# Performance work log

Measured on AMD Instinct MI355X. Metric: run time of the kernel, lower is better.

Reference implementation:

```python
import jax, jax.numpy as jnp
import numpy as np

GRID_H, GRID_W = 32, 32
THRESHOLD = 1.0
SMOOTH = 0.5


def setup_inputs() -> dict:
    key = jax.random.key(0)
    x = jax.random.normal(key, (64, GRID_H * GRID_W, 768), dtype=jnp.float32)
    return {"x": x}


def reference(x) -> jnp.ndarray:
    B, N, D = x.shape
    H, W = GRID_H, GRID_W
    xr = x.reshape(B, H, W, D)

    # L2 norm of neighbor differences (same as torch.norm(diff, dim=-1))
    diff_h = xr[:, :, 1:, :] - xr[:, :, :-1, :]            # [B, H, W-1, D]
    diff_v = xr[:, 1:, :, :] - xr[:, :-1, :, :]            # [B, H-1, W, D]
    anomaly_h = jnp.sqrt(jnp.sum(diff_h * diff_h, axis=-1))  # [B, H, W-1]
    anomaly_v = jnp.sqrt(jnp.sum(diff_v * diff_v, axis=-1))  # [B, H-1, W]

    # Torch code uses .any() over the batch dim: a patch is anomalous for ALL
    # batch elements if ANY batch element exceeds the threshold.
    exceed_h = jnp.any(anomaly_h > THRESHOLD, axis=0)      # [H, W-1]
    exceed_v = jnp.any(anomaly_v > THRESHOLD, axis=0)      # [H-1, W]

    # Interior patches: i in [1, H-2], j in [1, W-2].
    # Conditions checked per (i, j): ah[i, j-1], ah[i, j], av[i-1, j], av[i, j]
    mask = (exceed_h[1:H - 1, 0:W - 2]
            | exceed_h[1:H - 1, 1:W - 1]
            | exceed_v[0:H - 2, 1:W - 1]
            | exceed_v[1:H - 1, 1:W - 1])                  # [H-2, W-2]

    # 4-neighbor average (all reads from the ORIGINAL xr, as in the torch code)
    avg = (xr[:, 0:H - 2, 1:W - 1, :] + xr[:, 2:H, 1:W - 1, :]
           + xr[:, 1:H - 1, 0:W - 2, :] + xr[:, 1:H - 1, 2:W, :]) * 0.25

    center = xr[:, 1:H - 1, 1:W - 1, :]
    blended = (1.0 - SMOOTH) * center + SMOOTH * avg
    interior = jnp.where(mask[None, :, :, None], blended, center)

    out = xr.at[:, 1:H - 1, 1:W - 1, :].set(interior)
    return out.reshape(B, N, D)
```

## Files before the change

### kernel.cpp

```cpp
#include <hip/hip_runtime.h>

#define THRESH 1.0f

typedef float nfloat4 __attribute__((ext_vector_type(4)));

__device__ __forceinline__ float sqdiff4(float4 a, float4 b) {
  float dx = a.x - b.x, dy = a.y - b.y, dz = a.z - b.z, dw = a.w - b.w;
  return dx * dx + dy * dy + dz * dz + dw * dw;
}

__global__ __launch_bounds__(192) void mask_kernel(
    const float* __restrict__ x, int* __restrict__ mask) {
  const int n = blockIdx.x;
  const int i = n >> 5, j = n & 31;
  const int t = threadIdx.x;
  if (i < 1 || i > 30 || j < 1 || j > 30) {
    if (t == 0) mask[n] = 0;
    return;
  }
  __shared__ float red[3][4];
  __shared__ int sdone;
  if (t == 0) sdone = 0;
  __syncthreads();
  const int lane = t & 63;
  const int wid = t >> 6;
  const float4* xv = (const float4*)x;

  for (int b = 0; b < 64; ++b) {
    const size_t base = ((size_t)b * 1024 + n) * 192 + t;
    float4 c = xv[base];
    float4 l = xv[base - 192];
    float4 r = xv[base + 192];
    float4 u = xv[base - 32 * 192];
    float4 d = xv[base + 32 * 192];
    float sl = sqdiff4(c, l);
    float sr = sqdiff4(r, c);
    float su = sqdiff4(c, u);
    float sd = sqdiff4(d, c);
#pragma unroll
    for (int off = 32; off > 0; off >>= 1) {
      sl += __shfl_down(sl, off, 64);
      sr += __shfl_down(sr, off, 64);
      su += __shfl_down(su, off, 64);
      sd += __shfl_down(sd, off, 64);
    }
    if (lane == 0) {
      red[wid][0] = sl; red[wid][1] = sr;
      red[wid][2] = su; red[wid][3] = sd;
    }
    __syncthreads();
    if (t == 0) {
      float L = red[0][0] + red[1][0] + red[2][0];
      float R = red[0][1] + red[1][1] + red[2][1];
      float U = red[0][2] + red[1][2] + red[2][2];
      float D = red[0][3] + red[1][3] + red[2][3];
      if (L > THRESH || R > THRESH || U > THRESH || D > THRESH) sdone = 1;
    }
    __syncthreads();
    if (sdone) break;
  }
  if (t == 0) mask[n] = sdone;
}

__global__ __launch_bounds__(192) void apply_kernel(
    const float* __restrict__ x, const int* __restrict__ mask,
    float* __restrict__ out) {
  const int orig = blockIdx.x;
  const int bn = (orig & 7) * 8192 + (orig >> 3);
  const int n = bn & 1023;
  const int t = threadIdx.x;
  const size_t base = (size_t)bn * 192 + t;
  const float4* xv = (const float4*)x;
  nfloat4* ov = (nfloat4*)out;

  float4 c = xv[base];
  float4 res = c;
  if (mask[n]) {
    float4 l = xv[base - 192];
    float4 r = xv[base + 192];
    float4 u = xv[base - 32 * 192];
    float4 d = xv[base + 32 * 192];
    res.x = 0.5f * c.x + 0.125f * ((l.x + r.x) + (u.x + d.x));
    res.y = 0.5f * c.y + 0.125f * ((l.y + r.y) + (u.y + d.y));
    res.z = 0.5f * c.z + 0.125f * ((l.z + r.z) + (u.z + d.z));
    res.w = 0.5f * c.w + 0.125f * ((l.w + r.w) + (u.w + d.w));
  }
  nfloat4 nres = {res.x, res.y, res.z, res.w};
  __builtin_nontemporal_store(nres, ov + base);
}

extern "C" void kernel_launch(void* const* d_in, const int* in_sizes, int n_in,
                              void* d_out, int out_size, void* d_ws,
                              size_t ws_size, hipStream_t stream) {
  const float* x = (const float*)d_in[0];
  float* out = (float*)d_out;
  int* mask = (int*)d_ws;

  mask_kernel<<<1024, 192, 0, stream>>>(x, mask);
  apply_kernel<<<64 * 1024, 192, 0, stream>>>(x, mask, out);
}
```

Measured before the change: 348.2 us.

## Stream apply kernel down rows with register and shared-memory neighbor reuse

```diff
diff --git a/kernel.cpp b/kernel.cpp
--- a/kernel.cpp
+++ b/kernel.cpp
@@ -7,6 +7,11 @@
 __device__ __forceinline__ float sqdiff4(float4 a, float4 b) {
   float dx = a.x - b.x, dy = a.y - b.y, dz = a.z - b.z, dw = a.w - b.w;
   return dx * dx + dy * dy + dz * dz + dw * dw;
+}
+
+__device__ __forceinline__ nfloat4 to_n(float4 v) {
+  nfloat4 r = {v.x, v.y, v.z, v.w};
+  return r;
 }
 
 __global__ __launch_bounds__(192) void mask_kernel(
@@ -62,31 +67,104 @@
   if (t == 0) mask[n] = sdone;
 }
 
-__global__ __launch_bounds__(192) void apply_kernel(
+__global__ __launch_bounds__(512) void apply_kernel(
     const float* __restrict__ x, const int* __restrict__ mask,
     float* __restrict__ out) {
   const int orig = blockIdx.x;
-  const int bn = (orig & 7) * 8192 + (orig >> 3);
-  const int n = bn & 1023;
-  const int t = threadIdx.x;
-  const size_t base = (size_t)bn * 192 + t;
+  const int bn = (orig & 7) * 32 + (orig >> 3);
+  const int b  = bn >> 2;
+  const int jg = bn & 3;
+  const int t  = threadIdx.x;
+  const int cl = t >> 6;
+  const int k  = t & 63;
+  const int jglob = jg * 8 + cl;
+
+  __shared__ float4 row[10 * 192];
+
   const float4* xv = (const float4*)x;
   nfloat4* ov = (nfloat4*)out;
 
-  float4 c = xv[base];
-  float4 res = c;
-  if (mask[n]) {
-    float4 l = xv[base - 192];
-    float4 r = xv[base + 192];
-    float4 u = xv[base - 32 * 192];
-    float4 d = xv[base + 32 * 192];
-    res.x = 0.5f * c.x + 0.125f * ((l.x + r.x) + (u.x + d.x));
-    res.y = 0.5f * c.y + 0.125f * ((l.y + r.y) + (u.y + d.y));
-    res.z = 0.5f * c.z + 0.125f * ((l.z + r.z) + (u.z + d.z));
-    res.w = 0.5f * c.w + 0.125f * ((l.w + r.w) + (u.w + d.w));
+  const size_t batch_base = (size_t)b * 1024 * 192;
+  const int jL = (jg == 0) ? 0 : jg * 8 - 1;
+  const int jR = (jg == 3) ? 31 : jg * 8 + 8;
+  const bool haloT = (t < 384);
+  const int hj   = (t < 192) ? jL : jR;
+  const int hoff = (t < 192) ? t : (t - 192);
+  const int hslot = (t < 192) ? hoff : (9 * 192 + hoff);
+
+  float4 rU0, rU1, rU2, rC0, rC1, rC2, rD0, rD1, rD2, rN0, rN1, rN2;
+  float4 hC = {0, 0, 0, 0}, hN = {0, 0, 0, 0};
+
+  auto rowbase = [&](int i) -> size_t {
+    return batch_base + (size_t)(i * 32 + jglob) * 192 + k;
+  };
+  auto halobase = [&](int i) -> size_t {
+    return batch_base + (size_t)(i * 32 + hj) * 192 + hoff;
+  };
+
+  {
+    const size_t b0 = rowbase(0), b1 = rowbase(1), b2 = rowbase(2);
+    rU0 = xv[b0]; rU1 = xv[b0 + 64]; rU2 = xv[b0 + 128];
+    rC0 = xv[b1]; rC1 = xv[b1 + 64]; rC2 = xv[b1 + 128];
+    rD0 = xv[b2]; rD1 = xv[b2 + 64]; rD2 = xv[b2 + 128];
+    if (haloT) hC = xv[halobase(1)];
+    __builtin_nontemporal_store(to_n(rU0), ov + b0);
+    __builtin_nontemporal_store(to_n(rU1), ov + b0 + 64);
+    __builtin_nontemporal_store(to_n(rU2), ov + b0 + 128);
   }
-  nfloat4 nres = {res.x, res.y, res.z, res.w};
-  __builtin_nontemporal_store(nres, ov + base);
+
+  for (int i = 1; i <= 30; ++i) {
+    if (i <= 29) {
+      const size_t bnx = rowbase(i + 2);
+      rN0 = xv[bnx]; rN1 = xv[bnx + 64]; rN2 = xv[bnx + 128];
+      if (haloT) hN = xv[halobase(i + 1)];
+    }
+    __syncthreads();
+    row[(cl + 1) * 192 + k]       = rC0;
+    row[(cl + 1) * 192 + 64 + k]  = rC1;
+    row[(cl + 1) * 192 + 128 + k] = rC2;
+    if (haloT) row[hslot] = hC;
+    __syncthreads();
+
+    const int mv = mask[i * 32 + jglob];
+    const size_t ob = rowbase(i);
+    float4 res0 = rC0, res1 = rC1, res2 = rC2;
+    if (mv) {
+      const float4 l0 = row[cl * 192 + k];
+      const float4 l1 = row[cl * 192 + 64 + k];
+      const float4 l2 = row[cl * 192 + 128 + k];
+      const float4 r0 = row[(cl + 2) * 192 + k];
+      const float4 r1 = row[(cl + 2) * 192 + 64 + k];
+      const float4 r2 = row[(cl + 2) * 192 + 128 + k];
+      res0.x = 0.5f * rC0.x + 0.125f * ((l0.x + r0.x) + (rU0.x + rD0.x));
+      res0.y = 0.5f * rC0.y + 0.125f * ((l0.y + r0.y) + (rU0.y + rD0.y));
+      res0.z = 0.5f * rC0.z + 0.125f * ((l0.z + r0.z) + (rU0.z + rD0.z));
+      res0.w = 0.5f * rC0.w + 0.125f * ((l0.w + r0.w) + (rU0.w + rD0.w));
+      res1.x = 0.5f * rC1.x + 0.125f * ((l1.x + r1.x) + (rU1.x + rD1.x));
+      res1.y = 0.5f * rC1.y + 0.125f * ((l1.y + r1.y) + (rU1.y + rD1.y));
+      res1.z = 0.5f * rC1.z + 0.125f * ((l1.z + r1.z) + (rU1.z + rD1.z));
+      res1.w = 0.5f * rC1.w + 0.125f * ((l1.w + r1.w) + (rU1.w + rD1.w));
+      res2.x = 0.5f * rC2.x + 0.125f * ((l2.x + r2.x) + (rU2.x + rD2.x));
+      res2.y = 0.5f * rC2.y + 0.125f * ((l2.y + r2.y) + (rU2.y + rD2.y));
+      res2.z = 0.5f * rC2.z + 0.125f * ((l2.z + r2.z) + (rU2.z + rD2.z));
+      res2.w = 0.5f * rC2.w + 0.125f * ((l2.w + r2.w) + (rU2.w + rD2.w));
+    }
+    __builtin_nontemporal_store(to_n(res0), ov + ob);
+    __builtin_nontemporal_store(to_n(res1), ov + ob + 64);
+    __builtin_nontemporal_store(to_n(res2), ov + ob + 128);
+
+    rU0 = rC0; rU1 = rC1; rU2 = rC2;
+    rC0 = rD0; rC1 = rD1; rC2 = rD2;
+    rD0 = rN0; rD1 = rN1; rD2 = rN2;
+    hC = hN;
+  }
+
+  {
+    const size_t b31 = rowbase(31);
+    __builtin_nontemporal_store(to_n(rC0), ov + b31);
+    __builtin_nontemporal_store(to_n(rC1), ov + b31 + 64);
+    __builtin_nontemporal_store(to_n(rC2), ov + b31 + 128);
+  }
 }
 
 extern "C" void kernel_launch(void* const* d_in, const int* in_sizes, int n_in,
@@ -97,5 +175,5 @@
   int* mask = (int*)d_ws;
 
   mask_kernel<<<1024, 192, 0, stream>>>(x, mask);
-  apply_kernel<<<64 * 1024, 192, 0, stream>>>(x, mask, out);
+  apply_kernel<<<256, 512, 0, stream>>>(x, mask, out);
 }
```

New measurement: 346.4 us. No clear change (-0.5%).
